# Kernel tuning notes

Hardware: AMD Instinct MI355X
Metric: run time of the kernel (lower is better)

Reference implementation:

```python
import jax, jax.numpy as jnp
import numpy as np

B, T, N1, N2, D, H, DH = 8, 4, 1024, 64, 1024, 16, 64
INNER = H * DH
EPS = 1e-5


def layernorm(x, g, b):
    mu = jnp.mean(x, axis=-1, keepdims=True)
    var = jnp.var(x, axis=-1, keepdims=True)
    return (x - mu) * jax.lax.rsqrt(var + EPS) * g + b


def setup_inputs() -> dict:
    key = jax.random.key(0)
    ks = jax.random.split(key, 8)
    s = 0.02
    return {
        "x": jax.random.normal(ks[0], (B, T, N1, D), jnp.float32),
        "latents": jax.random.normal(ks[1], (B, T, N2, D), jnp.float32),
        "gm": jnp.ones((D,), jnp.float32),
        "bm": jnp.zeros((D,), jnp.float32),
        "gl": jnp.ones((D,), jnp.float32),
        "bl": jnp.zeros((D,), jnp.float32),
        "Wq": jax.random.normal(ks[2], (D, INNER), jnp.float32) * s,
        "Wkv": jax.random.normal(ks[3], (D, 2 * INNER), jnp.float32) * s,
        "Wout": jax.random.normal(ks[4], (INNER, D), jnp.float32) * s,
        "Wd1": jax.random.normal(ks[5], (D, D // 4), jnp.float32) * s,
        "bd1": jnp.zeros((D // 4,), jnp.float32),
        "Wd2": jax.random.normal(ks[6], (D // 4, H), jnp.float32) * s,
        "bd2": jnp.zeros((H,), jnp.float32),
    }


def reference(x, latents, gm, bm, gl, bl, Wq, Wkv, Wout, Wd1, bd1, Wd2, bd2):
    b, t, n1, d = x.shape
    n2 = latents.shape[2]
    h, dh = H, DH
    scale = dh ** -0.5

    xn = layernorm(x, gm, bm)
    ln = layernorm(latents, gl, bl)

    # q: (b, h, t, n2, dh)
    q = (ln @ Wq).reshape(b, t, n2, h, dh).transpose(0, 3, 1, 2, 4)
    # kv over image tokens + first latent token -> nk = n1 + 1
    kv_in = jnp.concatenate([xn, ln[:, :, 0:1]], axis=2)
    nk = n1 + 1
    kv = (kv_in @ Wkv).reshape(b, t, nk, 2, h, dh)
    k = kv[:, :, :, 0].transpose(0, 3, 1, 2, 4)  # (b, h, t, nk, dh)
    v = kv[:, :, :, 1].transpose(0, 3, 1, 2, 4)

    sim = jnp.einsum('bhtid,bhtjd->bhtij', q * scale, k)
    sim = sim - jax.lax.stop_gradient(jnp.max(sim, axis=-1, keepdims=True))
    attn = jax.nn.softmax(sim, axis=-1)

    # dynamic per-head weights from mean-pooled (normed) latents: (b, t, h)
    hid = jax.nn.relu(ln.mean(axis=2) @ Wd1 + bd1)
    dw = jax.nn.softmax(hid @ Wd2 + bd2, axis=-1)
    attn = attn * dw.transpose(0, 2, 1)[:, :, :, None, None]  # (b,h,t,1,1)

    out = jnp.einsum('bhtij,bhtjd->bhtid', attn, v)
    out = out.transpose(0, 2, 3, 1, 4).reshape(b, t, n2, h * dh)
    return out @ Wout
```

## Files before the change

### kernel.cpp

```cpp
#include <hip/hip_runtime.h>
#include <cstdint>
#include <cstddef>

constexpr int CB = 8, CT = 4, CN1 = 1024, CN2 = 64, CD = 1024, CH = 16, CDH = 64;
constexpr int CBT = CB * CT;
constexpr int CNK = CN1 + 1;
constexpr int CINNER = CH * CDH;

__device__ __forceinline__ unsigned short f2bf(float f) {
  union { float f; unsigned int u; } v; v.f = f;
  unsigned int u = v.u;
  u += 0x7fffu + ((u >> 16) & 1u);
  return (unsigned short)(u >> 16);
}

typedef __attribute__((ext_vector_type(8))) short short8;
typedef __attribute__((ext_vector_type(8))) __bf16 bf16x8;
typedef __attribute__((ext_vector_type(4))) float floatx4;

template <typename V>
__device__ __forceinline__ auto mfma_bf16_impl(V a, V b, floatx4 c, int)
    -> decltype(__builtin_amdgcn_mfma_f32_16x16x32_bf16(a, b, c, 0, 0, 0)) {
  return __builtin_amdgcn_mfma_f32_16x16x32_bf16(a, b, c, 0, 0, 0);
}
template <typename V>
__device__ __forceinline__ floatx4 mfma_bf16_impl(V a, V b, floatx4 c, long) {
  return __builtin_amdgcn_mfma_f32_16x16x32_bf16(
      __builtin_bit_cast(bf16x8, a), __builtin_bit_cast(bf16x8, b), c, 0, 0, 0);
}
__device__ __forceinline__ floatx4 mfma_bf16(short8 a, short8 b, floatx4 c) {
  return mfma_bf16_impl(a, b, c, 0);
}

#if __has_builtin(__builtin_amdgcn_global_load_lds)
#define HAS_GLDS 1
__device__ __forceinline__ void glds16(const unsigned short* g, unsigned short* l) {
  __builtin_amdgcn_global_load_lds(
      (const __attribute__((address_space(1))) void*)g,
      (__attribute__((address_space(3))) void*)l, 16, 0, 0);
}
#else
#define HAS_GLDS 0
#endif

__global__ __launch_bounds__(256) void ln_kernel(
    const float* __restrict__ x, const float* __restrict__ g,
    const float* __restrict__ b, unsigned short* __restrict__ obf,
    float* __restrict__ of32) {
  const int row = blockIdx.x * 4 + (threadIdx.x >> 6);
  const int lane = threadIdx.x & 63;
  const float4* xr = (const float4*)(x + (size_t)row * CD);
  float4 v[4];
#pragma unroll
  for (int k = 0; k < 4; ++k) v[k] = xr[lane + 64 * k];
  float s = 0.f, s2 = 0.f;
#pragma unroll
  for (int k = 0; k < 4; ++k) {
    s  += v[k].x + v[k].y + v[k].z + v[k].w;
    s2 += v[k].x*v[k].x + v[k].y*v[k].y + v[k].z*v[k].z + v[k].w*v[k].w;
  }
#pragma unroll
  for (int off = 32; off; off >>= 1) { s += __shfl_xor(s, off); s2 += __shfl_xor(s2, off); }
  const float mean = s * (1.0f / 1024.0f);
  const float var  = s2 * (1.0f / 1024.0f) - mean * mean;
  const float rstd = rsqrtf(var + 1e-5f);
#pragma unroll
  for (int k = 0; k < 4; ++k) {
    const float4 gv = ((const float4*)g)[lane + 64 * k];
    const float4 bv = ((const float4*)b)[lane + 64 * k];
    float4 y;
    y.x = (v[k].x - mean) * rstd * gv.x + bv.x;
    y.y = (v[k].y - mean) * rstd * gv.y + bv.y;
    y.z = (v[k].z - mean) * rstd * gv.z + bv.z;
    y.w = (v[k].w - mean) * rstd * gv.w + bv.w;
    ushort4 o; o.x = f2bf(y.x); o.y = f2bf(y.y); o.z = f2bf(y.z); o.w = f2bf(y.w);
    ((ushort4*)(obf + (size_t)row * CD))[lane + 64 * k] = o;
    if (of32) ((float4*)(of32 + (size_t)row * CD))[lane + 64 * k] = y;
  }
}

__global__ __launch_bounds__(256) void wtrans_kernel(
    const float* __restrict__ W, unsigned short* __restrict__ WT, int K, int N) {
  __shared__ float t[64][65];
  const int n0 = blockIdx.x * 64, k0 = blockIdx.y * 64;
  const int tid = threadIdx.x;
  const int kr = tid >> 4, ns = (tid & 15) * 4;
#pragma unroll
  for (int i = 0; i < 4; ++i) {
    const int k = kr + i * 16;
    const float4 v = *(const float4*)&W[(size_t)(k0 + k) * N + n0 + ns];
    t[k][ns + 0] = v.x; t[k][ns + 1] = v.y; t[k][ns + 2] = v.z; t[k][ns + 3] = v.w;
  }
  __syncthreads();
  const int n = tid >> 2, ks = (tid & 3) * 16;
#pragma unroll
  for (int c = 0; c < 4; ++c) {
    ushort4 o;
    o.x = f2bf(t[ks + c * 4 + 0][n]);
    o.y = f2bf(t[ks + c * 4 + 1][n]);
    o.z = f2bf(t[ks + c * 4 + 2][n]);
    o.w = f2bf(t[ks + c * 4 + 3][n]);
    *(ushort4*)&WT[(size_t)(n0 + n) * K + k0 + ks + c * 4] = o;
  }
}

template <bool A_KV, bool C_BF16>
__global__ __launch_bounds__(256) void gemm128_kernel(
    const unsigned short* __restrict__ A, const unsigned short* __restrict__ xn,
    const unsigned short* __restrict__ lnb, const unsigned short* __restrict__ BT,
    unsigned short* __restrict__ Cb, float* __restrict__ Cf,
    int M, int N, int K) {
  __shared__ __attribute__((aligned(16))) unsigned short As[128 * 32];
  __shared__ __attribute__((aligned(16))) unsigned short Bs[128 * 32];
  const int tid = threadIdx.x;
  const int col0 = blockIdx.x * 128, row0 = blockIdx.y * 128;
  const int srow = tid >> 2, skseg = (tid & 3) * 8;

  auto arow_ptr = [&](int grow) -> const unsigned short* {
    if (grow >= M) grow = M - 1;
    if (A_KV) {
      const int bt = grow / CNK, j = grow - bt * CNK;
      return (j < CN1) ? xn + ((size_t)(bt * CN1 + j)) * K + skseg
                       : lnb + ((size_t)(bt * CN2)) * K + skseg;
    }
    return A + (size_t)grow * K + skseg;
  };
  const unsigned short* a0 = arow_ptr(row0 + srow);
  const unsigned short* a1 = arow_ptr(row0 + 64 + srow);
  const unsigned short* b0 = BT + (size_t)(col0 + srow) * K + skseg;
  const unsigned short* b1 = BT + (size_t)(col0 + 64 + srow) * K + skseg;

  const int lane = tid & 63, wave = tid >> 6;
  const int wrow = (wave >> 1) * 64, wcol = (wave & 1) * 64;
  const int i16 = lane & 15, quad = lane >> 4;

  floatx4 acc[4][4] = {};
  for (int kt = 0; kt < K; kt += 32) {
    __syncthreads();
#if HAS_GLDS
    glds16(a0 + kt, &As[tid * 8]);
    glds16(a1 + kt, &As[2048 + tid * 8]);
    glds16(b0 + kt, &Bs[tid * 8]);
    glds16(b1 + kt, &Bs[2048 + tid * 8]);
#else
    *(uint4*)&As[tid * 8]        = *(const uint4*)(a0 + kt);
    *(uint4*)&As[2048 + tid * 8] = *(const uint4*)(a1 + kt);
    *(uint4*)&Bs[tid * 8]        = *(const uint4*)(b0 + kt);
    *(uint4*)&Bs[2048 + tid * 8] = *(const uint4*)(b1 + kt);
#endif
    __syncthreads();
    short8 af[4], bf[4];
#pragma unroll
    for (int ti = 0; ti < 4; ++ti)
      af[ti] = *(const short8*)&As[(wrow + ti * 16 + i16) * 32 + quad * 8];
#pragma unroll
    for (int tj = 0; tj < 4; ++tj)
      bf[tj] = *(const short8*)&Bs[(wcol + tj * 16 + i16) * 32 + quad * 8];
#pragma unroll
    for (int ti = 0; ti < 4; ++ti)
#pragma unroll
      for (int tj = 0; tj < 4; ++tj)
        acc[ti][tj] = mfma_bf16(af[ti], bf[tj], acc[ti][tj]);
  }
#pragma unroll
  for (int ti = 0; ti < 4; ++ti)
#pragma unroll
    for (int tj = 0; tj < 4; ++tj) {
      const int gc = col0 + wcol + tj * 16 + i16;
#pragma unroll
      for (int r = 0; r < 4; ++r) {
        const int gr = row0 + wrow + ti * 16 + quad * 4 + r;
        if (gr < M) {
          if (C_BF16) Cb[(size_t)gr * N + gc] = f2bf(acc[ti][tj][r]);
          else        Cf[(size_t)gr * N + gc] = acc[ti][tj][r];
        }
      }
    }
}

template <bool A_KV>
__global__ __launch_bounds__(512, 2) void gemm256_kernel(
    const unsigned short* __restrict__ A, const unsigned short* __restrict__ xn,
    const unsigned short* __restrict__ lnb, const unsigned short* __restrict__ BT,
    unsigned short* __restrict__ Cb,
    int M, int N, int K, int nbN) {
  __shared__ __attribute__((aligned(16))) unsigned short As[4 * 8192];
  __shared__ __attribute__((aligned(16))) unsigned short Bs[4 * 8192];
  const int tid = threadIdx.x;

  const int raw = blockIdx.x;
  const int cpx = gridDim.x >> 3;
  const int virt = (raw & 7) * cpx + (raw >> 3);
  const int mb = virt / nbN, nb = virt - mb * nbN;
  const int row0 = mb * 256, col0 = nb * 256;

  auto arow = [&](int grow) -> const unsigned short* {
    if (grow >= M) grow = M - 1;
    if (A_KV) {
      const int bt = grow / CNK, j = grow - bt * CNK;
      return (j < CN1) ? xn + ((size_t)(bt * CN1 + j)) * K
                       : lnb + ((size_t)(bt * CN2)) * K;
    }
    return A + (size_t)grow * K;
  };
  const int c0 = tid, c1 = tid + 512;
  const int rA0 = c0 >> 2, sA0 = (c0 & 3) ^ ((rA0 >> 1) & 3);
  const int rA1 = c1 >> 2, sA1 = (c1 & 3) ^ ((rA1 >> 1) & 3);
  const unsigned short* pA0 = arow(row0 + rA0) + sA0 * 8;
  const unsigned short* pA1 = arow(row0 + rA1) + sA1 * 8;
  const unsigned short* pB0 = BT + (size_t)(col0 + rA0) * K + sA0 * 8;
  const unsigned short* pB1 = BT + (size_t)(col0 + rA1) * K + sA1 * 8;

  auto stage = [&](int s) {
    const int sb = (s & 3) * 8192;
#if HAS_GLDS
    glds16(pA0 + s * 32, &As[sb + tid * 8]);
    glds16(pA1 + s * 32, &As[sb + 4096 + tid * 8]);
    glds16(pB0 + s * 32, &Bs[sb + tid * 8]);
    glds16(pB1 + s * 32, &Bs[sb + 4096 + tid * 8]);
#else
    *(uint4*)&As[sb + tid * 8]        = *(const uint4*)(pA0 + s * 32);
    *(uint4*)&As[sb + 4096 + tid * 8] = *(const uint4*)(pA1 + s * 32);
    *(uint4*)&Bs[sb + tid * 8]        = *(const uint4*)(pB0 + s * 32);
    *(uint4*)&Bs[sb + 4096 + tid * 8] = *(const uint4*)(pB1 + s * 32);
#endif
  };

  const int lane = tid & 63, wave = tid >> 6;
  const int wr = wave >> 2, wc = wave & 3;
  const int i16 = lane & 15, quad = lane >> 4;
  int offA[8], offB[4];
#pragma unroll
  for (int ti = 0; ti < 8; ++ti) {
    const int r = wr * 128 + ti * 16 + i16;
    offA[ti] = r * 32 + (quad ^ ((r >> 1) & 3)) * 8;
  }
#pragma unroll
  for (int tj = 0; tj < 4; ++tj) {
    const int r = wc * 64 + tj * 16 + i16;
    offB[tj] = r * 32 + (quad ^ ((r >> 1) & 3)) * 8;
  }

  floatx4 acc[8][4] = {};
  const int NSL = K >> 5;
  stage(0); stage(1); stage(2);

  auto phase = [&](int s, bool do_stage) {
    const unsigned short* Asl = &As[(s & 3) * 8192];
    const unsigned short* Bsl = &Bs[(s & 3) * 8192];
    if (do_stage) stage(s + 3);
    short8 bf[4];
#pragma unroll
    for (int tj = 0; tj < 4; ++tj) bf[tj] = *(const short8*)(Bsl + offB[tj]);
    short8 af[8];
    af[0] = *(const short8*)(Asl + offA[0]);
    af[1] = *(const short8*)(Asl + offA[1]);
    __builtin_amdgcn_s_setprio(1);
#pragma unroll
    for (int ti = 0; ti < 8; ++ti) {
      if (ti + 2 < 8) af[ti + 2] = *(const short8*)(Asl + offA[ti + 2]);
#pragma unroll
      for (int tj = 0; tj < 4; ++tj)
        acc[ti][tj] = mfma_bf16(af[ti], bf[tj], acc[ti][tj]);
    }
    __builtin_amdgcn_s_setprio(0);
  };

  for (int s = 0; s < NSL - 3; ++s) {
    asm volatile("s_waitcnt vmcnt(8)" ::: "memory");
    __builtin_amdgcn_s_barrier();
    __builtin_amdgcn_sched_barrier(0);
    phase(s, true);
  }
  asm volatile("s_waitcnt vmcnt(8)" ::: "memory");
  __builtin_amdgcn_s_barrier();
  __builtin_amdgcn_sched_barrier(0);
  phase(NSL - 3, false);
  asm volatile("s_waitcnt vmcnt(4)" ::: "memory");
  __builtin_amdgcn_s_barrier();
  __builtin_amdgcn_sched_barrier(0);
  phase(NSL - 2, false);
  asm volatile("s_waitcnt vmcnt(0)" ::: "memory");
  __builtin_amdgcn_s_barrier();
  __builtin_amdgcn_sched_barrier(0);
  phase(NSL - 1, false);

#pragma unroll
  for (int ti = 0; ti < 8; ++ti)
#pragma unroll
    for (int tj = 0; tj < 4; ++tj) {
      const int gc = col0 + wc * 64 + tj * 16 + i16;
#pragma unroll
      for (int r = 0; r < 4; ++r) {
        const int gr = row0 + wr * 128 + ti * 16 + quad * 4 + r;
        if (gr < M) Cb[(size_t)gr * N + gc] = f2bf(acc[ti][tj][r]);
      }
    }
}

__global__ __launch_bounds__(256) void dw_kernel(
    const float* __restrict__ lnf, const float* __restrict__ Wd1,
    const float* __restrict__ bd1, const float* __restrict__ Wd2,
    const float* __restrict__ bd2, float* __restrict__ dw) {
  __shared__ float mean[CD];
  __shared__ float hid[256];
  __shared__ float lg[16];
  const int bt = blockIdx.x, tid = threadIdx.x;
  const float* base = lnf + (size_t)bt * CN2 * CD;
  for (int d = tid; d < CD; d += 256) {
    float s = 0.f;
    for (int r = 0; r < CN2; ++r) s += base[(size_t)r * CD + d];
    mean[d] = s * (1.0f / 64.0f);
  }
  __syncthreads();
  {
    float s = bd1[tid];
    for (int d = 0; d < CD; ++d) s += mean[d] * Wd1[(size_t)d * 256 + tid];
    hid[tid] = fmaxf(s, 0.0f);
  }
  __syncthreads();
  if (tid < 16) {
    float s = bd2[tid];
    for (int o = 0; o < 256; ++o) s += hid[o] * Wd2[o * 16 + tid];
    lg[tid] = s;
  }
  __syncthreads();
  if (tid < 16) {
    float mx = lg[0];
    for (int h = 1; h < 16; ++h) mx = fmaxf(mx, lg[h]);
    float sum = 0.f;
    for (int h = 0; h < 16; ++h) sum += __expf(lg[h] - mx);
    dw[bt * 16 + tid] = __expf(lg[tid] - mx) / sum;
  }
}

__global__ __launch_bounds__(256) void attn_kernel(
    const unsigned short* __restrict__ Q,
    const unsigned short* __restrict__ KV,
    const float* __restrict__ dw,
    unsigned short* __restrict__ AO) {
  __shared__ __attribute__((aligned(16))) unsigned short ks[2][64 * 72];
  __shared__ __attribute__((aligned(16))) unsigned short vt[2][64 * 72];
  const int bt = blockIdx.x >> 4, h = blockIdx.x & 15;
  const int tid = threadIdx.x;
  const int lane = tid & 63, wave = tid >> 6;
  const int i16 = lane & 15, quad = lane >> 4;
  const int wrow = wave * 16;

  const unsigned short* qbase =
      Q + ((size_t)(bt * 64 + wrow + i16)) * CINNER + h * 64;
  const short8 bq0 = *(const short8*)(qbase + quad * 8);
  const short8 bq1 = *(const short8*)(qbase + 32 + quad * 8);

  const int jrb = tid & 31, seg = tid >> 5;
  const int t_ = jrb & 15, hlf_ = jrb >> 4;
  const int vcol0 = ((t_ >> 2) << 3) + (t_ & 3) + 4 * hlf_;
  const unsigned short* kvb = KV + ((size_t)bt * CNK) * 2048 + h * 64 + seg * 8;

  uint4 kk[2], vv[2];
  auto load_tile = [&](int j0) {
#pragma unroll
    for (int c = 0; c < 2; ++c) {
      const int j = j0 + c * 32 + jrb;
      if (j < CNK) {
        const unsigned short* p = kvb + (size_t)j * 2048;
        kk[c] = *(const uint4*)p;
        vv[c] = *(const uint4*)(p + 1024);
      } else {
        kk[c] = make_uint4(0, 0, 0, 0);
        vv[c] = make_uint4(0, 0, 0, 0);
      }
    }
  };
  auto write_tile = [&](int buf) {
#pragma unroll
    for (int c = 0; c < 2; ++c) {
      const int jr = c * 32 + jrb;
      *(uint4*)&ks[buf][jr * 72 + seg * 8] = kk[c];
      const int vcol = c * 32 + vcol0;
      const unsigned int w[4] = {vv[c].x, vv[c].y, vv[c].z, vv[c].w};
#pragma unroll
      for (int p = 0; p < 4; ++p) {
        vt[buf][(seg * 8 + 2 * p + 0) * 72 + vcol] = (unsigned short)(w[p] & 0xffffu);
        vt[buf][(seg * 8 + 2 * p + 1) * 72 + vcol] = (unsigned short)(w[p] >> 16);
      }
    }
  };

  float l = 0.f;
  floatx4 O[4] = {{0,0,0,0}, {0,0,0,0}, {0,0,0,0}, {0,0,0,0}};
  const float expC = 0.18033688011112042f;

  load_tile(0);
  write_tile(0);
  constexpr int NT = 17;
  for (int t = 0; t < NT; ++t) {
    if (t + 1 < NT) load_tile((t + 1) * 64);
    __syncthreads();
    const int buf = t & 1;
    const unsigned short* ksb = ks[buf];
    const unsigned short* vtb = vt[buf];
#pragma unroll
    for (int c = 0; c < 2; ++c) {
      floatx4 s0 = {0,0,0,0}, s1 = {0,0,0,0};
      const short8 a00 = *(const short8*)&ksb[((2*c)   * 16 + i16) * 72 + quad * 8];
      const short8 a01 = *(const short8*)&ksb[((2*c)   * 16 + i16) * 72 + 32 + quad * 8];
      const short8 a10 = *(const short8*)&ksb[((2*c+1) * 16 + i16) * 72 + quad * 8];
      const short8 a11 = *(const short8*)&ksb[((2*c+1) * 16 + i16) * 72 + 32 + quad * 8];
      s0 = mfma_bf16(a00, bq0, s0); s0 = mfma_bf16(a01, bq1, s0);
      s1 = mfma_bf16(a10, bq0, s1); s1 = mfma_bf16(a11, bq1, s1);
      unsigned short pb0[4], pb1[4];
      if (t == NT - 1) {
#pragma unroll
        for (int r = 0; r < 4; ++r) {
          const int k0g = t * 64 + (2*c)   * 16 + quad * 4 + r;
          const int k1g = t * 64 + (2*c+1) * 16 + quad * 4 + r;
          const float p0 = (k0g < CNK) ? exp2f(s0[r] * expC) : 0.f;
          const float p1 = (k1g < CNK) ? exp2f(s1[r] * expC) : 0.f;
          l += p0 + p1;
          pb0[r] = f2bf(p0); pb1[r] = f2bf(p1);
        }
      } else {
#pragma unroll
        for (int r = 0; r < 4; ++r) {
          const float p0 = exp2f(s0[r] * expC);
          const float p1 = exp2f(s1[r] * expC);
          l += p0 + p1;
          pb0[r] = f2bf(p0); pb1[r] = f2bf(p1);
        }
      }
      const short8 bp = {
          (short)pb0[0], (short)pb0[1], (short)pb0[2], (short)pb0[3],
          (short)pb1[0], (short)pb1[1], (short)pb1[2], (short)pb1[3]};
#pragma unroll
      for (int dt = 0; dt < 4; ++dt) {
        const short8 av = *(const short8*)&vtb[(dt * 16 + i16) * 72 + c * 32 + quad * 8];
        O[dt] = mfma_bf16(av, bp, O[dt]);
      }
    }
    if (t + 1 < NT) write_tile((t + 1) & 1);
  }

  l += __shfl_xor(l, 16);
  l += __shfl_xor(l, 32);
  const float wsc = dw[bt * 16 + h] / l;
  unsigned short* obase = AO + ((size_t)(bt * 64 + wrow + i16)) * CINNER + h * 64;
#pragma unroll
  for (int dt = 0; dt < 4; ++dt)
#pragma unroll
    for (int r = 0; r < 4; ++r)
      obase[dt * 16 + quad * 4 + r] = f2bf(O[dt][r] * wsc);
}

extern "C" void kernel_launch(void* const* d_in, const int* in_sizes, int n_in,
                              void* d_out, int out_size, void* d_ws, size_t ws_size,
                              hipStream_t stream) {
  const float* x       = (const float*)d_in[0];
  const float* latents = (const float*)d_in[1];
  const float* gm  = (const float*)d_in[2];
  const float* bm  = (const float*)d_in[3];
  const float* gl  = (const float*)d_in[4];
  const float* bl  = (const float*)d_in[5];
  const float* Wq  = (const float*)d_in[6];
  const float* Wkv = (const float*)d_in[7];
  const float* Wout= (const float*)d_in[8];
  const float* Wd1 = (const float*)d_in[9];
  const float* bd1 = (const float*)d_in[10];
  const float* Wd2 = (const float*)d_in[11];
  const float* bd2 = (const float*)d_in[12];
  float* out = (float*)d_out;

  char* ws = (char*)d_ws;
  size_t off = 0;
  auto alloc = [&](size_t bytes) -> void* {
    void* p = ws + off;
    off += (bytes + 255) & ~(size_t)255;
    return p;
  };
  unsigned short* xn   = (unsigned short*)alloc((size_t)CBT * CN1 * CD * 2);
  unsigned short* kv   = (unsigned short*)alloc((size_t)CBT * CNK * 2048 * 2);
  float*          lnf  = (float*)        alloc((size_t)CBT * CN2 * CD * 4);
  unsigned short* lnb  = (unsigned short*)alloc((size_t)CBT * CN2 * CD * 2);
  unsigned short* wqT  = (unsigned short*)alloc((size_t)CD * CINNER * 2);
  unsigned short* wkvT = (unsigned short*)alloc((size_t)CD * 2 * CINNER * 2);
  unsigned short* woT  = (unsigned short*)alloc((size_t)CINNER * CD * 2);
  unsigned short* qb   = (unsigned short*)alloc((size_t)CBT * CN2 * CINNER * 2);
  unsigned short* aob  = (unsigned short*)alloc((size_t)CBT * CN2 * CINNER * 2);
  float*          dwp  = (float*)        alloc((size_t)CBT * CH * 4);
  if (off > ws_size) return;

  ln_kernel<<<CBT * CN1 / 4, 256, 0, stream>>>(x, gm, bm, xn, nullptr);
  ln_kernel<<<CBT * CN2 / 4, 256, 0, stream>>>(latents, gl, bl, lnb, lnf);
  wtrans_kernel<<<dim3(CINNER / 64, CD / 64), 256, 0, stream>>>(Wq, wqT, CD, CINNER);
  wtrans_kernel<<<dim3(2 * CINNER / 64, CD / 64), 256, 0, stream>>>(Wkv, wkvT, CD, 2 * CINNER);
  wtrans_kernel<<<dim3(CD / 64, CINNER / 64), 256, 0, stream>>>(Wout, woT, CINNER, CD);
  gemm128_kernel<false, true><<<dim3(1024 / 128, 2048 / 128), 256, 0, stream>>>(
      lnb, nullptr, nullptr, wqT, qb, nullptr, 2048, 1024, 1024);
  {
    const int MB = (CBT * CNK + 255) / 256;
    gemm256_kernel<true><<<MB * 8, 512, 0, stream>>>(
        nullptr, xn, lnb, wkvT, kv, CBT * CNK, 2048, 1024, 8);
  }
  dw_kernel<<<CBT, 256, 0, stream>>>(lnf, Wd1, bd1, Wd2, bd2, dwp);
  attn_kernel<<<CBT * CH, 256, 0, stream>>>(qb, kv, dwp, aob);
  gemm128_kernel<false, false><<<dim3(1024 / 128, 2048 / 128), 256, 0, stream>>>(
      aob, nullptr, nullptr, woT, nullptr, out, 2048, 1024, 1024);
}
```

Before: 590.0 us.

## Shrink KV GEMM tiles to 128x128, split dynamic-weight MLP, remap attention blocks

After: 529.8 us. 1.11x faster.

```diff
diff --git a/kernel.cpp b/kernel.cpp
--- a/kernel.cpp
+++ b/kernel.cpp
@@ -179,20 +179,19 @@
 }
 
 template <bool A_KV>
-__global__ __launch_bounds__(512, 2) void gemm256_kernel(
-    const unsigned short* __restrict__ A, const unsigned short* __restrict__ xn,
-    const unsigned short* __restrict__ lnb, const unsigned short* __restrict__ BT,
-    unsigned short* __restrict__ Cb,
+__global__ __launch_bounds__(256) void gemmkv_kernel(
+    const unsigned short* __restrict__ xn, const unsigned short* __restrict__ lnb,
+    const unsigned short* __restrict__ BT, unsigned short* __restrict__ Cb,
     int M, int N, int K, int nbN) {
-  __shared__ __attribute__((aligned(16))) unsigned short As[4 * 8192];
-  __shared__ __attribute__((aligned(16))) unsigned short Bs[4 * 8192];
+  __shared__ __attribute__((aligned(16))) unsigned short As[3 * 4096];
+  __shared__ __attribute__((aligned(16))) unsigned short Bs[3 * 4096];
   const int tid = threadIdx.x;
 
   const int raw = blockIdx.x;
   const int cpx = gridDim.x >> 3;
   const int virt = (raw & 7) * cpx + (raw >> 3);
   const int mb = virt / nbN, nb = virt - mb * nbN;
-  const int row0 = mb * 256, col0 = nb * 256;
+  const int row0 = mb * 128, col0 = nb * 128;
 
   auto arow = [&](int grow) -> const unsigned short* {
     if (grow >= M) grow = M - 1;
@@ -201,9 +200,9 @@
       return (j < CN1) ? xn + ((size_t)(bt * CN1 + j)) * K
                        : lnb + ((size_t)(bt * CN2)) * K;
     }
-    return A + (size_t)grow * K;
-  };
-  const int c0 = tid, c1 = tid + 512;
+    return (const unsigned short*)nullptr;
+  };
+  const int c0 = tid, c1 = tid + 256;
   const int rA0 = c0 >> 2, sA0 = (c0 & 3) ^ ((rA0 >> 1) & 3);
   const int rA1 = c1 >> 2, sA1 = (c1 & 3) ^ ((rA1 >> 1) & 3);
   const unsigned short* pA0 = arow(row0 + rA0) + sA0 * 8;
@@ -212,27 +211,27 @@
   const unsigned short* pB1 = BT + (size_t)(col0 + rA1) * K + sA1 * 8;
 
   auto stage = [&](int s) {
-    const int sb = (s & 3) * 8192;
+    const int sb = (s % 3) * 4096;
 #if HAS_GLDS
     glds16(pA0 + s * 32, &As[sb + tid * 8]);
-    glds16(pA1 + s * 32, &As[sb + 4096 + tid * 8]);
+    glds16(pA1 + s * 32, &As[sb + 2048 + tid * 8]);
     glds16(pB0 + s * 32, &Bs[sb + tid * 8]);
-    glds16(pB1 + s * 32, &Bs[sb + 4096 + tid * 8]);
+    glds16(pB1 + s * 32, &Bs[sb + 2048 + tid * 8]);
 #else
     *(uint4*)&As[sb + tid * 8]        = *(const uint4*)(pA0 + s * 32);
-    *(uint4*)&As[sb + 4096 + tid * 8] = *(const uint4*)(pA1 + s * 32);
+    *(uint4*)&As[sb + 2048 + tid * 8] = *(const uint4*)(pA1 + s * 32);
     *(uint4*)&Bs[sb + tid * 8]        = *(const uint4*)(pB0 + s * 32);
-    *(uint4*)&Bs[sb + 4096 + tid * 8] = *(const uint4*)(pB1 + s * 32);
+    *(uint4*)&Bs[sb + 2048 + tid * 8] = *(const uint4*)(pB1 + s * 32);
 #endif
   };
 
   const int lane = tid & 63, wave = tid >> 6;
-  const int wr = wave >> 2, wc = wave & 3;
+  const int wr = wave >> 1, wc = wave & 1;
   const int i16 = lane & 15, quad = lane >> 4;
-  int offA[8], offB[4];
-#pragma unroll
-  for (int ti = 0; ti < 8; ++ti) {
-    const int r = wr * 128 + ti * 16 + i16;
+  int offA[4], offB[4];
+#pragma unroll
+  for (int ti = 0; ti < 4; ++ti) {
+    const int r = wr * 64 + ti * 16 + i16;
     offA[ti] = r * 32 + (quad ^ ((r >> 1) & 3)) * 8;
   }
 #pragma unroll
@@ -241,41 +240,34 @@
     offB[tj] = r * 32 + (quad ^ ((r >> 1) & 3)) * 8;
   }
 
-  floatx4 acc[8][4] = {};
+  floatx4 acc[4][4] = {};
   const int NSL = K >> 5;
-  stage(0); stage(1); stage(2);
+  stage(0); stage(1);
 
   auto phase = [&](int s, bool do_stage) {
-    const unsigned short* Asl = &As[(s & 3) * 8192];
-    const unsigned short* Bsl = &Bs[(s & 3) * 8192];
-    if (do_stage) stage(s + 3);
-    short8 bf[4];
+    const unsigned short* Asl = &As[(s % 3) * 4096];
+    const unsigned short* Bsl = &Bs[(s % 3) * 4096];
+    short8 bf[4], af[4];
 #pragma unroll
     for (int tj = 0; tj < 4; ++tj) bf[tj] = *(const short8*)(Bsl + offB[tj]);
-    short8 af[8];
-    af[0] = *(const short8*)(Asl + offA[0]);
-    af[1] = *(const short8*)(Asl + offA[1]);
+#pragma unroll
+    for (int ti = 0; ti < 4; ++ti) af[ti] = *(const short8*)(Asl + offA[ti]);
+    if (do_stage) stage(s + 2);
     __builtin_amdgcn_s_setprio(1);
 #pragma unroll
-    for (int ti = 0; ti < 8; ++ti) {
-      if (ti + 2 < 8) af[ti + 2] = *(const short8*)(Asl + offA[ti + 2]);
+    for (int ti = 0; ti < 4; ++ti)
 #pragma unroll
       for (int tj = 0; tj < 4; ++tj)
         acc[ti][tj] = mfma_bf16(af[ti], bf[tj], acc[ti][tj]);
-    }
     __builtin_amdgcn_s_setprio(0);
   };
 
-  for (int s = 0; s < NSL - 3; ++s) {
-    asm volatile("s_waitcnt vmcnt(8)" ::: "memory");
+  for (int s = 0; s < NSL - 2; ++s) {
+    asm volatile("s_waitcnt vmcnt(4)" ::: "memory");
     __builtin_amdgcn_s_barrier();
     __builtin_amdgcn_sched_barrier(0);
     phase(s, true);
   }
-  asm volatile("s_waitcnt vmcnt(8)" ::: "memory");
-  __builtin_amdgcn_s_barrier();
-  __builtin_amdgcn_sched_barrier(0);
-  phase(NSL - 3, false);
   asm volatile("s_waitcnt vmcnt(4)" ::: "memory");
   __builtin_amdgcn_s_barrier();
   __builtin_amdgcn_sched_barrier(0);
@@ -286,51 +278,80 @@
   phase(NSL - 1, false);
 
 #pragma unroll
-  for (int ti = 0; ti < 8; ++ti)
+  for (int ti = 0; ti < 4; ++ti)
 #pragma unroll
     for (int tj = 0; tj < 4; ++tj) {
       const int gc = col0 + wc * 64 + tj * 16 + i16;
 #pragma unroll
       for (int r = 0; r < 4; ++r) {
-        const int gr = row0 + wr * 128 + ti * 16 + quad * 4 + r;
+        const int gr = row0 + wr * 64 + ti * 16 + quad * 4 + r;
         if (gr < M) Cb[(size_t)gr * N + gc] = f2bf(acc[ti][tj][r]);
       }
     }
 }
 
-__global__ __launch_bounds__(256) void dw_kernel(
-    const float* __restrict__ lnf, const float* __restrict__ Wd1,
-    const float* __restrict__ bd1, const float* __restrict__ Wd2,
+__global__ __launch_bounds__(256) void dwmean_kernel(
+    const float* __restrict__ lnf, float* __restrict__ meanp) {
+  const int bt = blockIdx.x >> 2, dseg = blockIdx.x & 3;
+  const int d = dseg * 256 + threadIdx.x;
+  const float* base = lnf + (size_t)bt * CN2 * CD + d;
+  float s = 0.f;
+#pragma unroll 4
+  for (int r = 0; r < CN2; ++r) s += base[(size_t)r * CD];
+  meanp[bt * CD + d] = s * (1.0f / 64.0f);
+}
+
+__global__ __launch_bounds__(256) void dwmlp_kernel(
+    const float* __restrict__ meanp, const float* __restrict__ Wd1,
+    const float* __restrict__ bd1, float* __restrict__ hidp) {
+  __shared__ float red[8][32];
+  const int bt = blockIdx.x >> 3, og = blockIdx.x & 7;
+  const int o = threadIdx.x & 31, seg = threadIdx.x >> 5;
+  const int col = og * 32 + o;
+  const float* mb = meanp + bt * CD;
+  float s = 0.f;
+#pragma unroll 4
+  for (int d = seg * 128; d < seg * 128 + 128; ++d)
+    s += mb[d] * Wd1[(size_t)d * 256 + col];
+  red[seg][o] = s;
+  __syncthreads();
+  if (seg == 0) {
+    float t = red[0][o];
+#pragma unroll
+    for (int k = 1; k < 8; ++k) t += red[k][o];
+    hidp[bt * 256 + col] = fmaxf(t + bd1[col], 0.0f);
+  }
+}
+
+__global__ __launch_bounds__(256) void dwfin_kernel(
+    const float* __restrict__ hidp, const float* __restrict__ Wd2,
     const float* __restrict__ bd2, float* __restrict__ dw) {
-  __shared__ float mean[CD];
-  __shared__ float hid[256];
+  __shared__ float red[16][16];
   __shared__ float lg[16];
-  const int bt = blockIdx.x, tid = threadIdx.x;
-  const float* base = lnf + (size_t)bt * CN2 * CD;
-  for (int d = tid; d < CD; d += 256) {
-    float s = 0.f;
-    for (int r = 0; r < CN2; ++r) s += base[(size_t)r * CD + d];
-    mean[d] = s * (1.0f / 64.0f);
-  }
+  const int bt = blockIdx.x;
+  const int h = threadIdx.x & 15, seg = threadIdx.x >> 4;
+  const float* hb = hidp + bt * 256;
+  float s = 0.f;
+#pragma unroll
+  for (int o = seg * 16; o < seg * 16 + 16; ++o)
+    s += hb[o] * Wd2[o * 16 + h];
+  red[seg][h] = s;
   __syncthreads();
-  {
-    float s = bd1[tid];
-    for (int d = 0; d < CD; ++d) s += mean[d] * Wd1[(size_t)d * 256 + tid];
-    hid[tid] = fmaxf(s, 0.0f);
+  if (seg == 0) {
+    float t = red[0][h];
+#pragma unroll
+    for (int k = 1; k < 16; ++k) t += red[k][h];
+    lg[h] = t + bd2[h];
   }
   __syncthreads();
-  if (tid < 16) {
-    float s = bd2[tid];
-    for (int o = 0; o < 256; ++o) s += hid[o] * Wd2[o * 16 + tid];
-    lg[tid] = s;
-  }
-  __syncthreads();
-  if (tid < 16) {
+  if (threadIdx.x < 16) {
     float mx = lg[0];
-    for (int h = 1; h < 16; ++h) mx = fmaxf(mx, lg[h]);
+#pragma unroll
+    for (int k = 1; k < 16; ++k) mx = fmaxf(mx, lg[k]);
     float sum = 0.f;
-    for (int h = 0; h < 16; ++h) sum += __expf(lg[h] - mx);
-    dw[bt * 16 + tid] = __expf(lg[tid] - mx) / sum;
+#pragma unroll
+    for (int k = 0; k < 16; ++k) sum += __expf(lg[k] - mx);
+    dw[bt * 16 + threadIdx.x] = __expf(lg[threadIdx.x] - mx) / sum;
   }
 }
 
@@ -341,7 +362,9 @@
     unsigned short* __restrict__ AO) {
   __shared__ __attribute__((aligned(16))) unsigned short ks[2][64 * 72];
   __shared__ __attribute__((aligned(16))) unsigned short vt[2][64 * 72];
-  const int bt = blockIdx.x >> 4, h = blockIdx.x & 15;
+  const int raw = blockIdx.x;
+  const int bt = (raw & 7) * 4 + ((raw >> 3) >> 4);
+  const int h  = (raw >> 3) & 15;
   const int tid = threadIdx.x;
   const int lane = tid & 63, wave = tid >> 6;
   const int i16 = lane & 15, quad = lane >> 4;
@@ -487,6 +510,8 @@
   unsigned short* qb   = (unsigned short*)alloc((size_t)CBT * CN2 * CINNER * 2);
   unsigned short* aob  = (unsigned short*)alloc((size_t)CBT * CN2 * CINNER * 2);
   float*          dwp  = (float*)        alloc((size_t)CBT * CH * 4);
+  float*          meanp= (float*)        alloc((size_t)CBT * CD * 4);
+  float*          hidp = (float*)        alloc((size_t)CBT * 256 * 4);
   if (off > ws_size) return;
 
   ln_kernel<<<CBT * CN1 / 4, 256, 0, stream>>>(x, gm, bm, xn, nullptr);
@@ -497,11 +522,13 @@
   gemm128_kernel<false, true><<<dim3(1024 / 128, 2048 / 128), 256, 0, stream>>>(
       lnb, nullptr, nullptr, wqT, qb, nullptr, 2048, 1024, 1024);
   {
-    const int MB = (CBT * CNK + 255) / 256;
-    gemm256_kernel<true><<<MB * 8, 512, 0, stream>>>(
-        nullptr, xn, lnb, wkvT, kv, CBT * CNK, 2048, 1024, 8);
-  }
-  dw_kernel<<<CBT, 256, 0, stream>>>(lnf, Wd1, bd1, Wd2, bd2, dwp);
+    const int MB = (CBT * CNK + 127) / 128;
+    gemmkv_kernel<true><<<MB * 16, 256, 0, stream>>>(
+        xn, lnb, wkvT, kv, CBT * CNK, 2048, 1024, 16);
+  }
+  dwmean_kernel<<<CBT * 4, 256, 0, stream>>>(lnf, meanp);
+  dwmlp_kernel<<<CBT * 8, 256, 0, stream>>>(meanp, Wd1, bd1, hidp);
+  dwfin_kernel<<<CBT, 256, 0, stream>>>(hidp, Wd2, bd2, dwp);
   attn_kernel<<<CBT * CH, 256, 0, stream>>>(qb, kv, dwp, aob);
   gemm128_kernel<false, false><<<dim3(1024 / 128, 2048 / 128), 256, 0, stream>>>(
       aob, nullptr, nullptr, woT, nullptr, out, 2048, 1024, 1024);
```
